# Kernel optimization log

Measured on AMD Instinct MI355X. Metric: run time of the kernel, lower is better.

The kernel has to match this reference:

```python
import jax, jax.numpy as jnp
import numpy as np

N_EMBD = 1024
N_HEAD = 16
HEAD = N_EMBD // N_HEAD
B, T = 4, 2048


def setup_inputs() -> dict:
    key = jax.random.key(0)
    k1, k2, k3, k4, k5 = jax.random.split(key, 5)
    s = 1.0 / np.sqrt(N_EMBD)
    x = jax.random.normal(k1, (B, T, N_EMBD), dtype=jnp.float32)
    W_qkv = jax.random.uniform(k2, (N_EMBD, 3 * N_EMBD), jnp.float32, -s, s)
    b_qkv = jax.random.uniform(k3, (3 * N_EMBD,), jnp.float32, -s, s)
    W_out = jax.random.uniform(k4, (N_EMBD, N_EMBD), jnp.float32, -s, s)
    b_out = jax.random.uniform(k5, (N_EMBD,), jnp.float32, -s, s)
    return {"x": x, "W_qkv": W_qkv, "b_qkv": b_qkv, "W_out": W_out, "b_out": b_out}


def reference(x, W_qkv, b_qkv, W_out, b_out):
    Bx, Tx, C = x.shape
    qkv = x @ W_qkv + b_qkv                      # [B,T,3C]
    q, k, v = jnp.split(qkv, 3, axis=-1)
    def to_heads(t):
        return t.reshape(Bx, Tx, N_HEAD, HEAD).transpose(0, 2, 1, 3)  # [B,H,T,hd]
    q, k, v = to_heads(q), to_heads(k), to_heads(v)
    scores = jnp.einsum('bhqd,bhkd->bhqk', q, k) / np.sqrt(HEAD)
    causal = jnp.tril(jnp.ones((Tx, Tx), dtype=bool))
    scores = jnp.where(causal[None, None, :, :], scores, jnp.float32(-1e9))
    attn = jax.nn.softmax(scores, axis=-1)       # dropout p=0 (eval)
    out = jnp.einsum('bhqk,bhkd->bhqd', attn, v)
    out = out.transpose(0, 2, 1, 3).reshape(Bx, Tx, C)
    return out @ W_out + b_out
```

## Files before the change

kernel.cpp:

```cpp
#include <hip/hip_runtime.h>

typedef __attribute__((ext_vector_type(8))) short short8;
typedef __attribute__((ext_vector_type(8))) _Float16 half8;
typedef __attribute__((ext_vector_type(4))) float f32x4;
typedef __attribute__((ext_vector_type(16))) float f32x16;
typedef __attribute__((ext_vector_type(4))) unsigned uint4v;
typedef __attribute__((ext_vector_type(2))) float float2v;

#define MFMA_BF16(a, b, c) __builtin_amdgcn_mfma_f32_16x16x32_bf16(a, b, c, 0, 0, 0)
#define MFMA32_BF16(a, b, c) __builtin_amdgcn_mfma_f32_32x32x16_bf16(a, b, c, 0, 0, 0)
#define MFMA32_F16(a, b, c) __builtin_amdgcn_mfma_f32_32x32x16_f16(a, b, c, 0, 0, 0)

#define GLD16(g, l)                                                          \
  __builtin_amdgcn_global_load_lds(                                          \
      (const __attribute__((address_space(1))) unsigned int*)(g),            \
      (__attribute__((address_space(3))) unsigned int*)(l), 16, 0, 0)

__device__ __forceinline__ unsigned short f2bf(float f) {
  unsigned int u = __float_as_uint(f);
  u += 0x7fffu + ((u >> 16) & 1u);
  return (unsigned short)(u >> 16);
}

__global__ __launch_bounds__(256) void prep_k(const float* __restrict__ x,
                                              unsigned short* __restrict__ xb,
                                              const float* __restrict__ W_qkv,
                                              unsigned short* __restrict__ wqkvT,
                                              const float* __restrict__ W_out,
                                              unsigned short* __restrict__ woutT) {
  __shared__ float tile[64][65];
  const int blk = blockIdx.x;
  const int tid = threadIdx.x;
  if (blk < 8192) {
    int i = blk * 256 + tid;
    float4 v = reinterpret_cast<const float4*>(x)[i];
    ushort4 o;
    o.x = f2bf(v.x); o.y = f2bf(v.y); o.z = f2bf(v.z); o.w = f2bf(v.w);
    reinterpret_cast<ushort4*>(xb)[i] = o;
    return;
  }
  const float* W;
  unsigned short* Wt;
  int N, bx;
  if (blk < 8960) { W = W_qkv; Wt = wqkvT; N = 3072; bx = blk - 8192; }
  else            { W = W_out; Wt = woutT; N = 1024; bx = blk - 8960; }
  const int tk = (bx & 15) * 64;
  const int tn = (bx >> 4) * 64;
#pragma unroll
  for (int c = 0; c < 4; ++c) {
    int k = c * 16 + (tid >> 4);
    int n = (tid & 15) * 4;
    float4 v = *reinterpret_cast<const float4*>(&W[(size_t)(tk + k) * N + tn + n]);
    tile[k][n] = v.x; tile[k][n + 1] = v.y; tile[k][n + 2] = v.z; tile[k][n + 3] = v.w;
  }
  __syncthreads();
#pragma unroll
  for (int p = 0; p < 2; ++p) {
    int n = p * 32 + (tid >> 3);
    int k = (tid & 7) * 8;
    ushort4 a, b;
    a.x = f2bf(tile[k + 0][n]); a.y = f2bf(tile[k + 1][n]);
    a.z = f2bf(tile[k + 2][n]); a.w = f2bf(tile[k + 3][n]);
    b.x = f2bf(tile[k + 4][n]); b.y = f2bf(tile[k + 5][n]);
    b.z = f2bf(tile[k + 6][n]); b.w = f2bf(tile[k + 7][n]);
    *reinterpret_cast<ushort4*>(&Wt[(size_t)(tn + n) * 1024 + tk + k]) = a;
    *reinterpret_cast<ushort4*>(&Wt[(size_t)(tn + n) * 1024 + tk + k + 4]) = b;
  }
}

template <int MODE, int BN>
__global__ __launch_bounds__(256) void gemm_bt(const unsigned short* __restrict__ A,
                                               const unsigned short* __restrict__ Bt,
                                               const float* __restrict__ bias,
                                               float* __restrict__ outF,
                                               unsigned short* __restrict__ q_ws,
                                               unsigned short* __restrict__ k_ws,
                                               unsigned short* __restrict__ vt_ws,
                                               int M, int N, int K) {
  constexpr int NJ = BN / 32;
  constexpr int NBC = BN * 64 / 2048;
  __shared__ unsigned short As[128 * 64];
  __shared__ unsigned short Bs[BN * 64];

  const int tid = threadIdx.x;
  const int wave = tid >> 6, lane = tid & 63;
  const int quad = lane >> 4, l15 = lane & 15;
  const int m0 = blockIdx.x * 128, n0 = blockIdx.y * BN;
  const int wm = (wave & 1) * 64, wn = (wave >> 1) * (BN / 2);

  const f32x4 zf = {0.f, 0.f, 0.f, 0.f};
  f32x4 acc[4][NJ];
#pragma unroll
  for (int i = 0; i < 4; ++i)
#pragma unroll
    for (int j = 0; j < NJ; ++j) acc[i][j] = zf;

  const int rr = tid >> 3;
  const int scol = ((tid & 7) ^ (rr & 7)) * 8;
  const int swz = l15 & 7;

  for (int kt = 0; kt < K; kt += 64) {
    __syncthreads();
#pragma unroll
    for (int c = 0; c < 4; ++c)
      GLD16(&A[(size_t)(m0 + c * 32 + rr) * K + kt + scol], &As[c * 2048 + tid * 8]);
#pragma unroll
    for (int c = 0; c < NBC; ++c)
      GLD16(&Bt[(size_t)(n0 + c * 32 + rr) * K + kt + scol], &Bs[c * 2048 + tid * 8]);
    __syncthreads();

#pragma unroll
    for (int kk = 0; kk < 2; ++kk) {
      const int ch = (kk * 4 + quad) ^ swz;
      short8 af[4], bg[NJ];
#pragma unroll
      for (int i = 0; i < 4; ++i)
        af[i] = *reinterpret_cast<const short8*>(&As[(wm + i * 16 + l15) * 64 + ch * 8]);
#pragma unroll
      for (int j = 0; j < NJ; ++j)
        bg[j] = *reinterpret_cast<const short8*>(&Bs[(wn + j * 16 + l15) * 64 + ch * 8]);
#pragma unroll
      for (int i = 0; i < 4; ++i)
#pragma unroll
        for (int j = 0; j < NJ; ++j) acc[i][j] = MFMA_BF16(af[i], bg[j], acc[i][j]);
    }
  }

  const float kScQ = 0.125f * 1.44269504088896f;
  const int cls = n0 >> 10;
#pragma unroll
  for (int i = 0; i < 4; ++i) {
#pragma unroll
    for (int j = 0; j < NJ; ++j) {
      const int n = n0 + wn + j * 16 + l15;
      const float bv = bias[n];
      const int mb = m0 + wm + i * 16 + quad * 4;
      if (MODE == 1) {
#pragma unroll
        for (int r = 0; r < 4; ++r) outF[(size_t)(mb + r) * N + n] = acc[i][j][r] + bv;
      } else if (cls == 0) {
        const int b = mb >> 11, t0 = mb & 2047;
        const int h = n >> 6, d = n & 63;
#pragma unroll
        for (int r = 0; r < 4; ++r)
          q_ws[(((size_t)(b * 16 + h)) * 2048 + t0 + r) * 64 + d] =
              f2bf((acc[i][j][r] + bv) * kScQ);
      } else if (cls == 1) {
        const int b = mb >> 11, t0 = mb & 2047;
        const int n2 = n - 1024, h = n2 >> 6, d = n2 & 63;
#pragma unroll
        for (int r = 0; r < 4; ++r)
          k_ws[(((size_t)(b * 16 + h)) * 2048 + t0 + r) * 64 + d] = f2bf(acc[i][j][r] + bv);
      } else {
        const int b = mb >> 11, t0 = mb & 2047;
        const int n2 = n - 2048, h = n2 >> 6, d = n2 & 63;
        uint2 pk;
        pk.x = __builtin_bit_cast(unsigned int,
                                  __builtin_amdgcn_cvt_pkrtz(acc[i][j][0] + bv, acc[i][j][1] + bv));
        pk.y = __builtin_bit_cast(unsigned int,
                                  __builtin_amdgcn_cvt_pkrtz(acc[i][j][2] + bv, acc[i][j][3] + bv));
        *reinterpret_cast<uint2*>(
            &vt_ws[(((size_t)(b * 16 + h)) * 64 + d) * 2048 + t0]) = pk;
      }
    }
  }
}

__global__ __launch_bounds__(256, 3) void attn_k(const unsigned short* __restrict__ q_ws,
                                                 const unsigned short* __restrict__ k_ws,
                                                 const unsigned short* __restrict__ vt_ws,
                                                 unsigned short* __restrict__ att_ws) {
  const int T = 2048;
  const int bid = blockIdx.x;
  const int bh = (bid & 7) * 8 + ((bid >> 3) & 7);
  const int s = 15 - (bid >> 6);
  const int tid = threadIdx.x;
  const int wv = tid >> 6, lane = tid & 63;
  const int L = lane & 31, hl = lane >> 5;

  const unsigned short* Qh = q_ws + (size_t)bh * T * 64;
  const unsigned short* Kh = k_ws + (size_t)bh * T * 64;
  const _Float16* Vh = (const _Float16*)vt_ws + (size_t)bh * 64 * T;
  const int b = bh >> 4, h = bh & 15;

  __shared__ unsigned short Ks[2][64 * 64];
  __shared__ _Float16 Vs[2][64 * 64];

  const int qw = s * 4 + wv;
  const int q0 = qw * 32;
  const int diagTile = qw >> 1;
  const int nk = 2 * s + 2;
  const int myq = q0 + L;

  short8 qb[4];
#pragma unroll
  for (int kk = 0; kk < 4; ++kk)
    qb[kk] = *reinterpret_cast<const short8*>(&Qh[(size_t)(q0 + L) * 64 + kk * 16 + hl * 8]);

  f32x16 o0 = {}, o1 = {};
  float2v li = {0.f, 0.f};

  const int srow8 = tid >> 3;
  const int schunk = (tid & 7) ^ (srow8 & 7);

  GLD16(&Kh[(size_t)srow8 * 64 + schunk * 8], &Ks[0][tid * 8]);
  GLD16(&Kh[(size_t)(32 + srow8) * 64 + schunk * 8], &Ks[0][2048 + tid * 8]);
  GLD16(&Vh[(size_t)srow8 * T + schunk * 8], &Vs[0][tid * 8]);
  GLD16(&Vh[(size_t)(32 + srow8) * T + schunk * 8], &Vs[0][2048 + tid * 8]);

  auto softmax32 = [&](const f32x16& scc, unsigned (&pwc)[4][2]) {
#pragma unroll
    for (int g = 0; g < 4; ++g) {
      float2v e01, e23;
      e01[0] = exp2f(scc[4 * g + 0]);
      e01[1] = exp2f(scc[4 * g + 1]);
      e23[0] = exp2f(scc[4 * g + 2]);
      e23[1] = exp2f(scc[4 * g + 3]);
      float2v s2;
      asm("v_pk_add_f32 %0, %1, %2" : "=v"(s2) : "v"(e01), "v"(e23));
      asm("v_pk_add_f32 %0, %0, %1" : "+v"(li) : "v"(s2));
      pwc[g][0] = __builtin_bit_cast(unsigned int, __builtin_amdgcn_cvt_pkrtz(e01[0], e01[1]));
      pwc[g][1] = __builtin_bit_cast(unsigned int, __builtin_amdgcn_cvt_pkrtz(e23[0], e23[1]));
    }
#pragma unroll
    for (int r = 0; r < 2; ++r) {
      asm volatile("v_permlane32_swap_b32 %0, %1" : "+v"(pwc[0][r]), "+v"(pwc[1][r]));
      asm volatile("v_permlane32_swap_b32 %0, %1" : "+v"(pwc[2][r]), "+v"(pwc[3][r]));
    }
  };

  for (int kt = 0; kt < nk; ++kt) {
    const int cur = kt & 1, nxt = cur ^ 1;
    if (kt) asm volatile("s_barrier" ::: "memory");
    const int pf = (kt + 1 < nk) ? kt + 1 : nk - 1;
    GLD16(&Kh[(size_t)(pf * 64 + srow8) * 64 + schunk * 8], &Ks[nxt][tid * 8]);
    GLD16(&Kh[(size_t)(pf * 64 + 32 + srow8) * 64 + schunk * 8], &Ks[nxt][2048 + tid * 8]);
    GLD16(&Vh[(size_t)srow8 * T + pf * 64 + schunk * 8], &Vs[nxt][tid * 8]);
    GLD16(&Vh[(size_t)(32 + srow8) * T + pf * 64 + schunk * 8], &Vs[nxt][2048 + tid * 8]);
    asm volatile("s_waitcnt vmcnt(4)\n\ts_barrier" ::: "memory");

    if (kt <= diagTile) {
      const unsigned short* KsC = Ks[cur];
      const _Float16* VsC = Vs[cur];
      const int kb = kt * 64;

      f32x16 sc0 = {}, sc1 = {};
      __builtin_amdgcn_s_setprio(1);
#pragma unroll
      for (int kk = 0; kk < 4; ++kk) {
        const int sl = ((kk * 2 + hl) ^ (L & 7)) * 8;
        short8 k0 = *reinterpret_cast<const short8*>(&KsC[L * 64 + sl]);
        short8 k1 = *reinterpret_cast<const short8*>(&KsC[(32 + L) * 64 + sl]);
        sc0 = MFMA32_BF16(k0, qb[kk], sc0);
        sc1 = MFMA32_BF16(k1, qb[kk], sc1);
      }
      __builtin_amdgcn_s_setprio(0);

      half8 vr0[2], vr1[2];
#pragma unroll
      for (int t = 0; t < 2; ++t) {
        const int sl = ((t * 2 + hl) ^ (L & 7)) * 8;
        vr0[t] = *reinterpret_cast<const half8*>(&VsC[L * 64 + sl]);
        vr1[t] = *reinterpret_cast<const half8*>(&VsC[(32 + L) * 64 + sl]);
      }

      if (kt == diagTile) {
#pragma unroll
        for (int reg = 0; reg < 16; ++reg) {
          const int row = (reg & 3) + 8 * (reg >> 2) + 4 * hl;
          sc0[reg] = (kb + row > myq) ? -1e30f : sc0[reg];
        }
      }
      unsigned pw0[4][2], pw1[4][2];
      softmax32(sc0, pw0);

      half8 vr2[2], vr3[2];
#pragma unroll
      for (int t = 2; t < 4; ++t) {
        const int sl = ((t * 2 + hl) ^ (L & 7)) * 8;
        vr2[t - 2] = *reinterpret_cast<const half8*>(&VsC[L * 64 + sl]);
        vr3[t - 2] = *reinterpret_cast<const half8*>(&VsC[(32 + L) * 64 + sl]);
      }

      __builtin_amdgcn_s_setprio(1);
      {
        uint4v f0 = {pw0[0][0], pw0[0][1], pw0[1][0], pw0[1][1]};
        uint4v f1 = {pw0[2][0], pw0[2][1], pw0[3][0], pw0[3][1]};
        half8 pb0 = __builtin_bit_cast(half8, f0);
        half8 pb1 = __builtin_bit_cast(half8, f1);
        o0 = MFMA32_F16(vr0[0], pb0, o0);
        o1 = MFMA32_F16(vr1[0], pb0, o1);
        o0 = MFMA32_F16(vr0[1], pb1, o0);
        o1 = MFMA32_F16(vr1[1], pb1, o1);
      }
      __builtin_amdgcn_s_setprio(0);

      if (kt == diagTile) {
#pragma unroll
        for (int reg = 0; reg < 16; ++reg) {
          const int row = (reg & 3) + 8 * (reg >> 2) + 4 * hl;
          sc1[reg] = (kb + 32 + row > myq) ? -1e30f : sc1[reg];
        }
      }
      softmax32(sc1, pw1);

      __builtin_amdgcn_s_setprio(1);
      {
        uint4v f0 = {pw1[0][0], pw1[0][1], pw1[1][0], pw1[1][1]};
        uint4v f1 = {pw1[2][0], pw1[2][1], pw1[3][0], pw1[3][1]};
        half8 pb0 = __builtin_bit_cast(half8, f0);
        half8 pb1 = __builtin_bit_cast(half8, f1);
        o0 = MFMA32_F16(vr2[0], pb0, o0);
        o1 = MFMA32_F16(vr3[0], pb0, o1);
        o0 = MFMA32_F16(vr2[1], pb1, o0);
        o1 = MFMA32_F16(vr3[1], pb1, o1);
      }
      __builtin_amdgcn_s_setprio(0);
    }
  }
  asm volatile("s_waitcnt vmcnt(0)" ::: "memory");

  float l_i = li[0] + li[1];
  l_i += __shfl_xor(l_i, 32);
  const float inv = 1.f / l_i;
#pragma unroll
  for (int sg = 0; sg < 2; ++sg) {
    const f32x16& oo = sg ? o1 : o0;
#pragma unroll
    for (int g = 0; g < 4; ++g) {
      const int d0 = sg * 32 + g * 8 + hl * 4;
      uint2 ov;
      ov.x = (unsigned)f2bf(oo[4 * g + 0] * inv) | ((unsigned)f2bf(oo[4 * g + 1] * inv) << 16);
      ov.y = (unsigned)f2bf(oo[4 * g + 2] * inv) | ((unsigned)f2bf(oo[4 * g + 3] * inv) << 16);
      *reinterpret_cast<uint2*>(
          &att_ws[(size_t)(b * 2048 + q0 + L) * 1024 + h * 64 + d0]) = ov;
    }
  }
}

extern "C" void kernel_launch(void* const* d_in, const int* in_sizes, int n_in,
                              void* d_out, int out_size, void* d_ws, size_t ws_size,
                              hipStream_t stream) {
  (void)in_sizes; (void)n_in; (void)out_size; (void)ws_size;
  const float* x     = (const float*)d_in[0];
  const float* W_qkv = (const float*)d_in[1];
  const float* b_qkv = (const float*)d_in[2];
  const float* W_out = (const float*)d_in[3];
  const float* b_out = (const float*)d_in[4];
  float* out = (float*)d_out;

  char* ws = (char*)d_ws;
  unsigned short* xb    = (unsigned short*)(ws);
  unsigned short* wqkvT = (unsigned short*)(ws + 16777216);
  unsigned short* woutT = (unsigned short*)(ws + 23068672);
  unsigned short* q_ws  = (unsigned short*)(ws + 25165824);
  unsigned short* k_ws  = (unsigned short*)(ws + 41943040);
  unsigned short* vt_ws = (unsigned short*)(ws + 58720256);
  unsigned short* attb  = (unsigned short*)(ws + 75497472);

  prep_k<<<9216, 256, 0, stream>>>(x, xb, W_qkv, wqkvT, W_out, woutT);

  dim3 g1(64, 24);
  gemm_bt<0, 128><<<g1, 256, 0, stream>>>(xb, wqkvT, b_qkv, nullptr, q_ws, k_ws, vt_ws,
                                          8192, 3072, 1024);
  attn_k<<<1024, 256, 0, stream>>>(q_ws, k_ws, vt_ws, attb);

  dim3 g2(64, 16);
  gemm_bt<1, 64><<<g2, 256, 0, stream>>>(attb, woutT, b_out, out, nullptr, nullptr, nullptr,
                                         8192, 1024, 1024);
}
```

Baseline: 247.9 us.

## Load K/V fragments directly from global memory instead of LDS staging

The attention kernel drops the double-buffered LDS staging of K and V tiles, along with its barriers and async global-to-LDS copies. Each wave now reads its own K and V MFMA fragments straight from global memory and runs only up to its own diagonal tile. This removes block-level synchronisation and lets waves with fewer tiles finish early. The cost is that the four waves in a block each fetch the same K/V data separately, so the kernel relies on cache hits, and the loads are no longer prefetched a tile ahead.

```diff
diff --git a/kernel.cpp b/kernel.cpp
--- a/kernel.cpp
+++ b/kernel.cpp
@@ -183,13 +183,9 @@
   const _Float16* Vh = (const _Float16*)vt_ws + (size_t)bh * 64 * T;
   const int b = bh >> 4, h = bh & 15;
 
-  __shared__ unsigned short Ks[2][64 * 64];
-  __shared__ _Float16 Vs[2][64 * 64];
-
   const int qw = s * 4 + wv;
   const int q0 = qw * 32;
   const int diagTile = qw >> 1;
-  const int nk = 2 * s + 2;
   const int myq = q0 + L;
 
   short8 qb[4];
@@ -200,13 +196,10 @@
   f32x16 o0 = {}, o1 = {};
   float2v li = {0.f, 0.f};
 
-  const int srow8 = tid >> 3;
-  const int schunk = (tid & 7) ^ (srow8 & 7);
-
-  GLD16(&Kh[(size_t)srow8 * 64 + schunk * 8], &Ks[0][tid * 8]);
-  GLD16(&Kh[(size_t)(32 + srow8) * 64 + schunk * 8], &Ks[0][2048 + tid * 8]);
-  GLD16(&Vh[(size_t)srow8 * T + schunk * 8], &Vs[0][tid * 8]);
-  GLD16(&Vh[(size_t)(32 + srow8) * T + schunk * 8], &Vs[0][2048 + tid * 8]);
+  const unsigned short* Kp0 = Kh + (size_t)L * 64 + hl * 8;
+  const unsigned short* Kp1 = Kh + (size_t)(32 + L) * 64 + hl * 8;
+  const _Float16* Vp0 = Vh + (size_t)L * T + hl * 8;
+  const _Float16* Vp1 = Vh + (size_t)(32 + L) * T + hl * 8;
 
   auto softmax32 = [&](const f32x16& scc, unsigned (&pwc)[4][2]) {
 #pragma unroll
@@ -229,96 +222,79 @@
     }
   };
 
-  for (int kt = 0; kt < nk; ++kt) {
-    const int cur = kt & 1, nxt = cur ^ 1;
-    if (kt) asm volatile("s_barrier" ::: "memory");
-    const int pf = (kt + 1 < nk) ? kt + 1 : nk - 1;
-    GLD16(&Kh[(size_t)(pf * 64 + srow8) * 64 + schunk * 8], &Ks[nxt][tid * 8]);
-    GLD16(&Kh[(size_t)(pf * 64 + 32 + srow8) * 64 + schunk * 8], &Ks[nxt][2048 + tid * 8]);
-    GLD16(&Vh[(size_t)srow8 * T + pf * 64 + schunk * 8], &Vs[nxt][tid * 8]);
-    GLD16(&Vh[(size_t)(32 + srow8) * T + pf * 64 + schunk * 8], &Vs[nxt][2048 + tid * 8]);
-    asm volatile("s_waitcnt vmcnt(4)\n\ts_barrier" ::: "memory");
-
-    if (kt <= diagTile) {
-      const unsigned short* KsC = Ks[cur];
-      const _Float16* VsC = Vs[cur];
-      const int kb = kt * 64;
-
-      f32x16 sc0 = {}, sc1 = {};
-      __builtin_amdgcn_s_setprio(1);
-#pragma unroll
-      for (int kk = 0; kk < 4; ++kk) {
-        const int sl = ((kk * 2 + hl) ^ (L & 7)) * 8;
-        short8 k0 = *reinterpret_cast<const short8*>(&KsC[L * 64 + sl]);
-        short8 k1 = *reinterpret_cast<const short8*>(&KsC[(32 + L) * 64 + sl]);
-        sc0 = MFMA32_BF16(k0, qb[kk], sc0);
-        sc1 = MFMA32_BF16(k1, qb[kk], sc1);
+  for (int kt = 0; kt <= diagTile; ++kt) {
+    const int kb = kt * 64;
+
+    short8 kf0[4], kf1[4];
+#pragma unroll
+    for (int kk = 0; kk < 4; ++kk) {
+      kf0[kk] = *reinterpret_cast<const short8*>(Kp0 + (size_t)kb * 64 + kk * 16);
+      kf1[kk] = *reinterpret_cast<const short8*>(Kp1 + (size_t)kb * 64 + kk * 16);
+    }
+    half8 v00 = *reinterpret_cast<const half8*>(Vp0 + kb);
+    half8 v10 = *reinterpret_cast<const half8*>(Vp1 + kb);
+    half8 v01 = *reinterpret_cast<const half8*>(Vp0 + kb + 16);
+    half8 v11 = *reinterpret_cast<const half8*>(Vp1 + kb + 16);
+
+    f32x16 sc0 = {}, sc1 = {};
+    __builtin_amdgcn_s_setprio(1);
+#pragma unroll
+    for (int kk = 0; kk < 4; ++kk) {
+      sc0 = MFMA32_BF16(kf0[kk], qb[kk], sc0);
+      sc1 = MFMA32_BF16(kf1[kk], qb[kk], sc1);
+    }
+    __builtin_amdgcn_s_setprio(0);
+
+    half8 v02 = *reinterpret_cast<const half8*>(Vp0 + kb + 32);
+    half8 v12 = *reinterpret_cast<const half8*>(Vp1 + kb + 32);
+    half8 v03 = *reinterpret_cast<const half8*>(Vp0 + kb + 48);
+    half8 v13 = *reinterpret_cast<const half8*>(Vp1 + kb + 48);
+
+    if (kt == diagTile) {
+#pragma unroll
+      for (int reg = 0; reg < 16; ++reg) {
+        const int row = (reg & 3) + 8 * (reg >> 2) + 4 * hl;
+        sc0[reg] = (kb + row > myq) ? -1e30f : sc0[reg];
       }
-      __builtin_amdgcn_s_setprio(0);
-
-      half8 vr0[2], vr1[2];
-#pragma unroll
-      for (int t = 0; t < 2; ++t) {
-        const int sl = ((t * 2 + hl) ^ (L & 7)) * 8;
-        vr0[t] = *reinterpret_cast<const half8*>(&VsC[L * 64 + sl]);
-        vr1[t] = *reinterpret_cast<const half8*>(&VsC[(32 + L) * 64 + sl]);
+    }
+    unsigned pw0[4][2], pw1[4][2];
+    softmax32(sc0, pw0);
+
+    __builtin_amdgcn_s_setprio(1);
+    {
+      uint4v f0 = {pw0[0][0], pw0[0][1], pw0[1][0], pw0[1][1]};
+      uint4v f1 = {pw0[2][0], pw0[2][1], pw0[3][0], pw0[3][1]};
+      half8 pb0 = __builtin_bit_cast(half8, f0);
+      half8 pb1 = __builtin_bit_cast(half8, f1);
+      o0 = MFMA32_F16(v00, pb0, o0);
+      o1 = MFMA32_F16(v10, pb0, o1);
+      o0 = MFMA32_F16(v01, pb1, o0);
+      o1 = MFMA32_F16(v11, pb1, o1);
+    }
+    __builtin_amdgcn_s_setprio(0);
+
+    if (kt == diagTile) {
+#pragma unroll
+      for (int reg = 0; reg < 16; ++reg) {
+        const int row = (reg & 3) + 8 * (reg >> 2) + 4 * hl;
+        sc1[reg] = (kb + 32 + row > myq) ? -1e30f : sc1[reg];
       }
-
-      if (kt == diagTile) {
-#pragma unroll
-        for (int reg = 0; reg < 16; ++reg) {
-          const int row = (reg & 3) + 8 * (reg >> 2) + 4 * hl;
-          sc0[reg] = (kb + row > myq) ? -1e30f : sc0[reg];
-        }
-      }
-      unsigned pw0[4][2], pw1[4][2];
-      softmax32(sc0, pw0);
-
-      half8 vr2[2], vr3[2];
-#pragma unroll
-      for (int t = 2; t < 4; ++t) {
-        const int sl = ((t * 2 + hl) ^ (L & 7)) * 8;
-        vr2[t - 2] = *reinterpret_cast<const half8*>(&VsC[L * 64 + sl]);
-        vr3[t - 2] = *reinterpret_cast<const half8*>(&VsC[(32 + L) * 64 + sl]);
-      }
-
-      __builtin_amdgcn_s_setprio(1);
-      {
-        uint4v f0 = {pw0[0][0], pw0[0][1], pw0[1][0], pw0[1][1]};
-        uint4v f1 = {pw0[2][0], pw0[2][1], pw0[3][0], pw0[3][1]};
-        half8 pb0 = __builtin_bit_cast(half8, f0);
-        half8 pb1 = __builtin_bit_cast(half8, f1);
-        o0 = MFMA32_F16(vr0[0], pb0, o0);
-        o1 = MFMA32_F16(vr1[0], pb0, o1);
-        o0 = MFMA32_F16(vr0[1], pb1, o0);
-        o1 = MFMA32_F16(vr1[1], pb1, o1);
-      }
-      __builtin_amdgcn_s_setprio(0);
-
-      if (kt == diagTile) {
-#pragma unroll
-        for (int reg = 0; reg < 16; ++reg) {
-          const int row = (reg & 3) + 8 * (reg >> 2) + 4 * hl;
-          sc1[reg] = (kb + 32 + row > myq) ? -1e30f : sc1[reg];
-        }
-      }
-      softmax32(sc1, pw1);
-
-      __builtin_amdgcn_s_setprio(1);
-      {
-        uint4v f0 = {pw1[0][0], pw1[0][1], pw1[1][0], pw1[1][1]};
-        uint4v f1 = {pw1[2][0], pw1[2][1], pw1[3][0], pw1[3][1]};
-        half8 pb0 = __builtin_bit_cast(half8, f0);
-        half8 pb1 = __builtin_bit_cast(half8, f1);
-        o0 = MFMA32_F16(vr2[0], pb0, o0);
-        o1 = MFMA32_F16(vr3[0], pb0, o1);
-        o0 = MFMA32_F16(vr2[1], pb1, o0);
-        o1 = MFMA32_F16(vr3[1], pb1, o1);
-      }
-      __builtin_amdgcn_s_setprio(0);
-    }
-  }
-  asm volatile("s_waitcnt vmcnt(0)" ::: "memory");
+    }
+    softmax32(sc1, pw1);
+
+    __builtin_amdgcn_s_setprio(1);
+    {
+      uint4v f0 = {pw1[0][0], pw1[0][1], pw1[1][0], pw1[1][1]};
+      uint4v f1 = {pw1[2][0], pw1[2][1], pw1[3][0], pw1[3][1]};
+      half8 pb0 = __builtin_bit_cast(half8, f0);
+      half8 pb1 = __builtin_bit_cast(half8, f1);
+      o0 = MFMA32_F16(v02, pb0, o0);
+      o1 = MFMA32_F16(v12, pb0, o1);
+      o0 = MFMA32_F16(v03, pb1, o0);
+      o1 = MFMA32_F16(v13, pb1, o1);
+    }
+    __builtin_amdgcn_s_setprio(0);
+  }
 
   float l_i = li[0] + li[1];
   l_i += __shfl_xor(l_i, 32);
```

Result: slower. 319.2 us (+28.8%).

## Double-buffer GEMM with 512-thread 128x256 tiles and use raw exp2 in softmax

Applied to the files above, without the earlier changes.

Replaces the 256-thread GEMM with a 512-thread kernel using 128x256 tiles and double-buffered LDS, so the global-to-LDS load of the next K tile overlaps the MFMA work on the current one. It waits with a partial vmcnt and raises wave priority around the MFMA block. Both the QKV and output projections use it with fewer, larger blocks. The attention softmax now calls the hardware exp2 builtin instead of exp2f. The cost is more LDS per block (96KB) and fewer blocks for the output GEMM (256), which may underfill the GPU.

```diff
diff --git a/kernel.cpp b/kernel.cpp
--- a/kernel.cpp
+++ b/kernel.cpp
@@ -68,70 +68,83 @@
   }
 }
 
-template <int MODE, int BN>
-__global__ __launch_bounds__(256) void gemm_bt(const unsigned short* __restrict__ A,
-                                               const unsigned short* __restrict__ Bt,
-                                               const float* __restrict__ bias,
-                                               float* __restrict__ outF,
-                                               unsigned short* __restrict__ q_ws,
-                                               unsigned short* __restrict__ k_ws,
-                                               unsigned short* __restrict__ vt_ws,
-                                               int M, int N, int K) {
-  constexpr int NJ = BN / 32;
-  constexpr int NBC = BN * 64 / 2048;
-  __shared__ unsigned short As[128 * 64];
-  __shared__ unsigned short Bs[BN * 64];
-
+template <int MODE>
+__global__ __launch_bounds__(512, 2) void gemm8(const unsigned short* __restrict__ A,
+                                                const unsigned short* __restrict__ Bt,
+                                                const float* __restrict__ bias,
+                                                float* __restrict__ outF,
+                                                unsigned short* __restrict__ q_ws,
+                                                unsigned short* __restrict__ k_ws,
+                                                unsigned short* __restrict__ vt_ws,
+                                                int N) {
+  constexpr int K = 1024;
+  __shared__ unsigned short As[2][128 * 64];
+  __shared__ unsigned short Bs[2][256 * 64];
   const int tid = threadIdx.x;
   const int wave = tid >> 6, lane = tid & 63;
   const int quad = lane >> 4, l15 = lane & 15;
-  const int m0 = blockIdx.x * 128, n0 = blockIdx.y * BN;
-  const int wm = (wave & 1) * 64, wn = (wave >> 1) * (BN / 2);
+  const int m0 = blockIdx.x * 128, n0 = blockIdx.y * 256;
+  const int wm = (wave & 1) * 64, wn = (wave >> 1) * 64;
 
   const f32x4 zf = {0.f, 0.f, 0.f, 0.f};
-  f32x4 acc[4][NJ];
+  f32x4 acc[4][4];
 #pragma unroll
   for (int i = 0; i < 4; ++i)
 #pragma unroll
-    for (int j = 0; j < NJ; ++j) acc[i][j] = zf;
+    for (int j = 0; j < 4; ++j) acc[i][j] = zf;
 
   const int rr = tid >> 3;
   const int scol = ((tid & 7) ^ (rr & 7)) * 8;
   const int swz = l15 & 7;
-
-  for (int kt = 0; kt < K; kt += 64) {
-    __syncthreads();
+  const unsigned short* Arow = &A[(size_t)(m0 + rr) * K + scol];
+  const unsigned short* Brow = &Bt[(size_t)(n0 + rr) * K + scol];
+
+#pragma unroll
+  for (int c = 0; c < 2; ++c)
+    GLD16(Arow + (size_t)c * 64 * K, &As[0][c * 4096 + tid * 8]);
+#pragma unroll
+  for (int c = 0; c < 4; ++c)
+    GLD16(Brow + (size_t)c * 64 * K, &Bs[0][c * 4096 + tid * 8]);
+
+  for (int t = 0; t < 16; ++t) {
+    const int cur = t & 1, nxt = cur ^ 1;
+    const int pf = (t < 15) ? (t + 1) : 15;
+    const size_t ko = (size_t)pf * 64;
+#pragma unroll
+    for (int c = 0; c < 2; ++c)
+      GLD16(Arow + (size_t)c * 64 * K + ko, &As[nxt][c * 4096 + tid * 8]);
 #pragma unroll
     for (int c = 0; c < 4; ++c)
-      GLD16(&A[(size_t)(m0 + c * 32 + rr) * K + kt + scol], &As[c * 2048 + tid * 8]);
-#pragma unroll
-    for (int c = 0; c < NBC; ++c)
-      GLD16(&Bt[(size_t)(n0 + c * 32 + rr) * K + kt + scol], &Bs[c * 2048 + tid * 8]);
-    __syncthreads();
+      GLD16(Brow + (size_t)c * 64 * K + ko, &Bs[nxt][c * 4096 + tid * 8]);
+    asm volatile("s_waitcnt vmcnt(6)\n\ts_barrier" ::: "memory");
 
 #pragma unroll
     for (int kk = 0; kk < 2; ++kk) {
       const int ch = (kk * 4 + quad) ^ swz;
-      short8 af[4], bg[NJ];
+      short8 af[4], bg[4];
 #pragma unroll
       for (int i = 0; i < 4; ++i)
-        af[i] = *reinterpret_cast<const short8*>(&As[(wm + i * 16 + l15) * 64 + ch * 8]);
-#pragma unroll
-      for (int j = 0; j < NJ; ++j)
-        bg[j] = *reinterpret_cast<const short8*>(&Bs[(wn + j * 16 + l15) * 64 + ch * 8]);
+        af[i] = *reinterpret_cast<const short8*>(&As[cur][(wm + i * 16 + l15) * 64 + ch * 8]);
+#pragma unroll
+      for (int j = 0; j < 4; ++j)
+        bg[j] = *reinterpret_cast<const short8*>(&Bs[cur][(wn + j * 16 + l15) * 64 + ch * 8]);
+      __builtin_amdgcn_s_setprio(1);
 #pragma unroll
       for (int i = 0; i < 4; ++i)
 #pragma unroll
-        for (int j = 0; j < NJ; ++j) acc[i][j] = MFMA_BF16(af[i], bg[j], acc[i][j]);
-    }
-  }
+        for (int j = 0; j < 4; ++j) acc[i][j] = MFMA_BF16(af[i], bg[j], acc[i][j]);
+      __builtin_amdgcn_s_setprio(0);
+      asm volatile("s_barrier" ::: "memory");
+    }
+  }
+  asm volatile("s_waitcnt vmcnt(0)" ::: "memory");
 
   const float kScQ = 0.125f * 1.44269504088896f;
   const int cls = n0 >> 10;
 #pragma unroll
   for (int i = 0; i < 4; ++i) {
 #pragma unroll
-    for (int j = 0; j < NJ; ++j) {
+    for (int j = 0; j < 4; ++j) {
       const int n = n0 + wn + j * 16 + l15;
       const float bv = bias[n];
       const int mb = m0 + wm + i * 16 + quad * 4;
@@ -212,10 +225,10 @@
 #pragma unroll
     for (int g = 0; g < 4; ++g) {
       float2v e01, e23;
-      e01[0] = exp2f(scc[4 * g + 0]);
-      e01[1] = exp2f(scc[4 * g + 1]);
-      e23[0] = exp2f(scc[4 * g + 2]);
-      e23[1] = exp2f(scc[4 * g + 3]);
+      e01[0] = __builtin_amdgcn_exp2f(scc[4 * g + 0]);
+      e01[1] = __builtin_amdgcn_exp2f(scc[4 * g + 1]);
+      e23[0] = __builtin_amdgcn_exp2f(scc[4 * g + 2]);
+      e23[1] = __builtin_amdgcn_exp2f(scc[4 * g + 3]);
       float2v s2;
       asm("v_pk_add_f32 %0, %1, %2" : "=v"(s2) : "v"(e01), "v"(e23));
       asm("v_pk_add_f32 %0, %0, %1" : "+v"(li) : "v"(s2));
@@ -360,12 +373,11 @@
 
   prep_k<<<9216, 256, 0, stream>>>(x, xb, W_qkv, wqkvT, W_out, woutT);
 
-  dim3 g1(64, 24);
-  gemm_bt<0, 128><<<g1, 256, 0, stream>>>(xb, wqkvT, b_qkv, nullptr, q_ws, k_ws, vt_ws,
-                                          8192, 3072, 1024);
+  dim3 g1(64, 12);
+  gemm8<0><<<g1, 512, 0, stream>>>(xb, wqkvT, b_qkv, nullptr, q_ws, k_ws, vt_ws, 3072);
+
   attn_k<<<1024, 256, 0, stream>>>(q_ws, k_ws, vt_ws, attb);
 
-  dim3 g2(64, 16);
-  gemm_bt<1, 64><<<g2, 256, 0, stream>>>(attb, woutT, b_out, out, nullptr, nullptr, nullptr,
-                                         8192, 1024, 1024);
-}
+  dim3 g2(64, 4);
+  gemm8<1><<<g2, 512, 0, stream>>>(attb, woutT, b_out, out, nullptr, nullptr, nullptr, 1024);
+}
```

Result: no change. 246.1 us (-0.7%).

## Double-buffer GEMM LDS tiles with prefetch and widen out-projection tile

Applied to the files above, without the earlier changes.

The GEMM kernel now keeps two LDS buffers for the A and B tiles. It issues the global_load_lds for tile t+1 before computing on tile t, and uses s_waitcnt vmcnt(8) plus s_barrier in place of the two __syncthreads per K step. The goal is to hide global-load latency behind the MFMA work. MFMA sections are wrapped in s_setprio, the output projection moves from BN=64 to BN=128 with half the grid columns, and the softmax exp2f calls become the raw __builtin_amdgcn_exp2f. The trade-offs are double the LDS use, which may lower occupancy, a hand-counted vmcnt that only holds for the 8-loads-per-iteration configuration, and fewer blocks in the out-projection.

```diff
diff --git a/kernel.cpp b/kernel.cpp
--- a/kernel.cpp
+++ b/kernel.cpp
@@ -69,7 +69,7 @@
 }
 
 template <int MODE, int BN>
-__global__ __launch_bounds__(256) void gemm_bt(const unsigned short* __restrict__ A,
+__global__ __launch_bounds__(256) void gemm_db(const unsigned short* __restrict__ A,
                                                const unsigned short* __restrict__ Bt,
                                                const float* __restrict__ bias,
                                                float* __restrict__ outF,
@@ -79,8 +79,8 @@
                                                int M, int N, int K) {
   constexpr int NJ = BN / 32;
   constexpr int NBC = BN * 64 / 2048;
-  __shared__ unsigned short As[128 * 64];
-  __shared__ unsigned short Bs[BN * 64];
+  __shared__ unsigned short As[2][128 * 64];
+  __shared__ unsigned short Bs[2][BN * 64];
 
   const int tid = threadIdx.x;
   const int wave = tid >> 6, lane = tid & 63;
@@ -98,16 +98,25 @@
   const int rr = tid >> 3;
   const int scol = ((tid & 7) ^ (rr & 7)) * 8;
   const int swz = l15 & 7;
-
-  for (int kt = 0; kt < K; kt += 64) {
-    __syncthreads();
+  const int nt = K >> 6;
+
+#pragma unroll
+  for (int c = 0; c < 4; ++c)
+    GLD16(&A[(size_t)(m0 + c * 32 + rr) * K + scol], &As[0][c * 2048 + tid * 8]);
+#pragma unroll
+  for (int c = 0; c < NBC; ++c)
+    GLD16(&Bt[(size_t)(n0 + c * 32 + rr) * K + scol], &Bs[0][c * 2048 + tid * 8]);
+
+  for (int t = 0; t < nt; ++t) {
+    const int cur = t & 1, nxt = cur ^ 1;
+    const int ko = ((t + 1 < nt) ? t + 1 : nt - 1) * 64;
 #pragma unroll
     for (int c = 0; c < 4; ++c)
-      GLD16(&A[(size_t)(m0 + c * 32 + rr) * K + kt + scol], &As[c * 2048 + tid * 8]);
+      GLD16(&A[(size_t)(m0 + c * 32 + rr) * K + ko + scol], &As[nxt][c * 2048 + tid * 8]);
 #pragma unroll
     for (int c = 0; c < NBC; ++c)
-      GLD16(&Bt[(size_t)(n0 + c * 32 + rr) * K + kt + scol], &Bs[c * 2048 + tid * 8]);
-    __syncthreads();
+      GLD16(&Bt[(size_t)(n0 + c * 32 + rr) * K + ko + scol], &Bs[nxt][c * 2048 + tid * 8]);
+    asm volatile("s_waitcnt vmcnt(8)\n\ts_barrier" ::: "memory");
 
 #pragma unroll
     for (int kk = 0; kk < 2; ++kk) {
@@ -115,16 +124,20 @@
       short8 af[4], bg[NJ];
 #pragma unroll
       for (int i = 0; i < 4; ++i)
-        af[i] = *reinterpret_cast<const short8*>(&As[(wm + i * 16 + l15) * 64 + ch * 8]);
+        af[i] = *reinterpret_cast<const short8*>(&As[cur][(wm + i * 16 + l15) * 64 + ch * 8]);
 #pragma unroll
       for (int j = 0; j < NJ; ++j)
-        bg[j] = *reinterpret_cast<const short8*>(&Bs[(wn + j * 16 + l15) * 64 + ch * 8]);
+        bg[j] = *reinterpret_cast<const short8*>(&Bs[cur][(wn + j * 16 + l15) * 64 + ch * 8]);
+      __builtin_amdgcn_s_setprio(1);
 #pragma unroll
       for (int i = 0; i < 4; ++i)
 #pragma unroll
         for (int j = 0; j < NJ; ++j) acc[i][j] = MFMA_BF16(af[i], bg[j], acc[i][j]);
-    }
-  }
+      __builtin_amdgcn_s_setprio(0);
+    }
+    asm volatile("s_barrier" ::: "memory");
+  }
+  asm volatile("s_waitcnt vmcnt(0)" ::: "memory");
 
   const float kScQ = 0.125f * 1.44269504088896f;
   const int cls = n0 >> 10;
@@ -212,10 +225,10 @@
 #pragma unroll
     for (int g = 0; g < 4; ++g) {
       float2v e01, e23;
-      e01[0] = exp2f(scc[4 * g + 0]);
-      e01[1] = exp2f(scc[4 * g + 1]);
-      e23[0] = exp2f(scc[4 * g + 2]);
-      e23[1] = exp2f(scc[4 * g + 3]);
+      e01[0] = __builtin_amdgcn_exp2f(scc[4 * g + 0]);
+      e01[1] = __builtin_amdgcn_exp2f(scc[4 * g + 1]);
+      e23[0] = __builtin_amdgcn_exp2f(scc[4 * g + 2]);
+      e23[1] = __builtin_amdgcn_exp2f(scc[4 * g + 3]);
       float2v s2;
       asm("v_pk_add_f32 %0, %1, %2" : "=v"(s2) : "v"(e01), "v"(e23));
       asm("v_pk_add_f32 %0, %0, %1" : "+v"(li) : "v"(s2));
@@ -361,11 +374,12 @@
   prep_k<<<9216, 256, 0, stream>>>(x, xb, W_qkv, wqkvT, W_out, woutT);
 
   dim3 g1(64, 24);
-  gemm_bt<0, 128><<<g1, 256, 0, stream>>>(xb, wqkvT, b_qkv, nullptr, q_ws, k_ws, vt_ws,
+  gemm_db<0, 128><<<g1, 256, 0, stream>>>(xb, wqkvT, b_qkv, nullptr, q_ws, k_ws, vt_ws,
                                           8192, 3072, 1024);
+
   attn_k<<<1024, 256, 0, stream>>>(q_ws, k_ws, vt_ws, attb);
 
-  dim3 g2(64, 16);
-  gemm_bt<1, 64><<<g2, 256, 0, stream>>>(attb, woutT, b_out, out, nullptr, nullptr, nullptr,
-                                         8192, 1024, 1024);
-}
+  dim3 g2(64, 8);
+  gemm_db<1, 128><<<g2, 256, 0, stream>>>(attb, woutT, b_out, out, nullptr, nullptr, nullptr,
+                                          8192, 1024, 1024);
+}
```

Result: faster. 239.0 us (-3.6%).
